# Optimization experiments

Hardware: AMD Instinct MI355X
Metric: run time of the kernel (lower is better)

## Reference

```python
import jax, jax.numpy as jnp
import numpy as np

B, J, D = 512, 22, 3
HIDDEN = 512
OUT = J * D          # 66, flattened frame size
NCLS = 12
LENGTH = 64


def setup_inputs() -> dict:
    key = jax.random.key(0)
    ks = jax.random.split(key, 12)
    s = 0.05
    return {
        "inputs": jax.random.normal(ks[0], (B, J, D), dtype=jnp.float32),
        "labels": jax.random.randint(ks[1], (B,), 0, NCLS),
        "length": LENGTH,
        # LSTMCell params (torch layout: W_ih [4H, in], W_hh [4H, H], gate order i,f,g,o)
        "W_ih": jax.random.normal(ks[2], (4 * HIDDEN, OUT + NCLS), dtype=jnp.float32) * s,
        "W_hh": jax.random.normal(ks[3], (4 * HIDDEN, HIDDEN), dtype=jnp.float32) * s,
        "b_ih": jax.random.normal(ks[4], (4 * HIDDEN,), dtype=jnp.float32) * s,
        "b_hh": jax.random.normal(ks[5], (4 * HIDDEN,), dtype=jnp.float32) * s,
        # fc: hidden -> output
        "W_fc": jax.random.normal(ks[6], (OUT, HIDDEN), dtype=jnp.float32) * s,
        "b_fc": jax.random.normal(ks[7], (OUT,), dtype=jnp.float32) * s,
        # fc_inh / fc_inc: output -> hidden (initial state projections)
        "W_inh": jax.random.normal(ks[8], (HIDDEN, OUT), dtype=jnp.float32) * s,
        "b_inh": jax.random.normal(ks[9], (HIDDEN,), dtype=jnp.float32) * s,
        "W_inc": jax.random.normal(ks[10], (HIDDEN, OUT), dtype=jnp.float32) * s,
        "b_inc": jax.random.normal(ks[11], (HIDDEN,), dtype=jnp.float32) * s,
    }


def reference(inputs, labels, length, W_ih, W_hh, b_ih, b_hh, W_fc, b_fc,
              W_inh, b_inh, W_inc, b_inc):
    b, j, d = inputs.shape
    enc = jax.nn.one_hot(labels, NCLS, dtype=inputs.dtype)      # [B, NCLS]
    frame0 = inputs.reshape(b, j * d)                            # [B, OUT]
    h0 = frame0 @ W_inh.T + b_inh                                # [B, H]
    c0 = frame0 @ W_inc.T + b_inc                                # [B, H]
    frame = jnp.concatenate([frame0, enc], axis=-1)              # [B, OUT+NCLS]

    def step(carry, _):
        h, c, fr = carry
        gates = fr @ W_ih.T + b_ih + h @ W_hh.T + b_hh           # [B, 4H]
        i, f, g, o = jnp.split(gates, 4, axis=-1)                # torch gate order
        c_new = jax.nn.sigmoid(f) * c + jax.nn.sigmoid(i) * jnp.tanh(g)
        h_new = jax.nn.sigmoid(o) * jnp.tanh(c_new)
        out = h_new @ W_fc.T + b_fc                              # [B, OUT]
        fr_new = jnp.concatenate([out, enc], axis=-1)
        return (h_new, c_new, fr_new), out

    _, outs = jax.lax.scan(step, (h0, c0, frame), None, length=length)  # [L, B, OUT]
    return jnp.transpose(outs, (1, 0, 2)).reshape(b, length, j, d)
```

## Files before the change

### kernel.cpp

```cpp
#include <hip/hip_runtime.h>

#define OUTD 66
#define INW  78
#define FH   2048
#define LEN  64

typedef short bf16x8 __attribute__((ext_vector_type(8)));
typedef float f32x4  __attribute__((ext_vector_type(4)));
typedef unsigned int u32x4 __attribute__((ext_vector_type(4)));

__device__ __forceinline__ float bf2f(unsigned short u) {
  union { unsigned int i; float f; } v; v.i = ((unsigned int)u) << 16; return v.f;
}
__device__ __forceinline__ unsigned short f2bf(float f) {
  union { float f; unsigned int i; } v; v.f = f;
  unsigned int u = v.i;
  return (unsigned short)((u + 0x7fffu + ((u >> 16) & 1u)) >> 16);
}
__device__ __forceinline__ float sigm(float x) { return 1.f / (1.f + __expf(-x)); }
__device__ __forceinline__ float tanh_f(float x) { return 2.f / (1.f + __expf(-2.f * x)) - 1.f; }

__device__ __forceinline__ unsigned int atom_add_ret(unsigned int* p, unsigned int d) {
  unsigned int r;
  asm volatile("global_atomic_add %0, %1, %2, off sc0\n\ts_waitcnt vmcnt(0)"
               : "=&v"(r) : "v"(p), "v"(d) : "memory");
  return r;
}

__global__ __launch_bounds__(256) void k_initA(
    const float* __restrict__ W_hh, const float* __restrict__ W_ih,
    const float* __restrict__ W_fc, const float* __restrict__ b_ih,
    const float* __restrict__ b_hh, const float* __restrict__ b_fc,
    const float* __restrict__ inp, const float* __restrict__ W_inh,
    const float* __restrict__ b_inh, const float* __restrict__ W_inc,
    const float* __restrict__ b_inc,
    unsigned short* __restrict__ Weff, float* __restrict__ bias_eff,
    unsigned short* __restrict__ hbuf, float* __restrict__ c0,
    unsigned short* __restrict__ Wfc16, unsigned int* __restrict__ flags,
    unsigned int* __restrict__ flagsL)
{
  int tid = threadIdx.x, bid = blockIdx.x;
  if (bid < 256) {
    int nb = bid;
    int k = tid * 2;
    float acc[8][2];
    #pragma unroll
    for (int r = 0; r < 8; ++r) {
      int n = nb * 8 + r;
      acc[r][0] = W_hh[n * 512 + k];
      acc[r][1] = W_hh[n * 512 + k + 1];
    }
    for (int m = 0; m < OUTD; ++m) {
      float w0 = W_fc[m * 512 + k];
      float w1 = W_fc[m * 512 + k + 1];
      #pragma unroll
      for (int r = 0; r < 8; ++r) {
        float wih = W_ih[(nb * 8 + r) * INW + m];
        acc[r][0] += wih * w0;
        acc[r][1] += wih * w1;
      }
    }
    #pragma unroll
    for (int r = 0; r < 8; ++r) {
      int n = nb * 8 + r;
      unsigned int pack = (unsigned int)f2bf(acc[r][0]) | ((unsigned int)f2bf(acc[r][1]) << 16);
      *(unsigned int*)(Weff + n * 512 + k) = pack;
    }
    if (tid < 8) {
      int n = nb * 8 + tid;
      float a = b_ih[n] + b_hh[n];
      for (int m = 0; m < OUTD; ++m) a += b_fc[m] * W_ih[n * INW + m];
      bias_eff[n] = a;
    }
    if (nb == 0) {
      for (int i = tid; i < 512 * 16; i += 256) flags[i] = 0;
      for (int i = tid; i < 256 * 16; i += 256) flagsL[i] = 0;
    }
  } else {
    int nb = bid - 256;
    for (int r = 0; r < 2; ++r) {
      int b = nb * 2 + r;
      for (int half = 0; half < 2; ++half) {
        int c = tid + half * 256;
        float ha = b_inh[c], ca = b_inc[c];
        for (int m = 0; m < OUTD; ++m) {
          float f = inp[b * OUTD + m];
          ha += f * W_inh[c * OUTD + m];
          ca += f * W_inc[c * OUTD + m];
        }
        hbuf[((b >> 5) * 32 + (c >> 4)) * 512 + (b & 31) * 16 + (c & 15)] = f2bf(ha);
        c0[b * 512 + c] = ca;
      }
    }
    if (nb == 0) {
      for (int i = tid; i < OUTD * 512; i += 256) Wfc16[i] = f2bf(W_fc[i]);
    }
  }
}

__global__ __launch_bounds__(128) void k_init2a(
    const float* __restrict__ inp, const unsigned short* __restrict__ hbuf,
    const float* __restrict__ W_fc, const float* __restrict__ b_fc,
    float* __restrict__ d0)
{
  int b = blockIdx.x, m = threadIdx.x;
  if (m >= OUTD) return;
  const unsigned short* hb = hbuf + (b >> 5) * 16384 + (b & 31) * 16;
  const float* wrow = W_fc + m * 512;
  float acc = 0.f;
  for (int k = 0; k < 512; ++k)
    acc += bf2f(hb[(k >> 4) * 512 + (k & 15)]) * wrow[k];
  d0[b * OUTD + m] = inp[b * OUTD + m] - (acc + b_fc[m]);
}

__global__ __launch_bounds__(256) void k_init2b(
    const float* __restrict__ d0, const float* __restrict__ W_ih,
    float* __restrict__ corr0)
{
  __shared__ float ds[4][OUTD];
  int tid = threadIdx.x, b0 = blockIdx.x * 4;
  for (int i = tid; i < 4 * OUTD; i += 256) ds[i / OUTD][i % OUTD] = d0[b0 * OUTD + i];
  __syncthreads();
  for (int n = tid; n < FH; n += 256) {
    float a0 = 0, a1 = 0, a2 = 0, a3 = 0;
    const float* wr = W_ih + n * INW;
    for (int m = 0; m < OUTD; ++m) {
      float w = wr[m];
      a0 += ds[0][m] * w; a1 += ds[1][m] * w; a2 += ds[2][m] * w; a3 += ds[3][m] * w;
    }
    corr0[(b0 + 0) * FH + n] = a0;
    corr0[(b0 + 1) * FH + n] = a1;
    corr0[(b0 + 2) * FH + n] = a2;
    corr0[(b0 + 3) * FH + n] = a3;
  }
}

__global__ __launch_bounds__(256, 2) void k_main(
    const unsigned short* __restrict__ Weff, const float* __restrict__ bias_eff,
    unsigned short* __restrict__ hbuf, const float* __restrict__ c0,
    const float* __restrict__ corr0, const float* __restrict__ W_ih,
    const int* __restrict__ labels, const unsigned short* __restrict__ Wfc16,
    const float* __restrict__ b_fc, float* __restrict__ out,
    unsigned int* __restrict__ flags, unsigned int* __restrict__ flagsL)
{
  __shared__ __align__(16) unsigned short h_lds[32 * 512];

  int tid = threadIdx.x, bid = blockIdx.x;
  int w = tid >> 6, lane = tid & 63;
  int lc = lane & 15, kg = lane >> 4;
  unsigned int* xmap = flags + 4608;
  unsigned int* decp = flags + 4100;

  unsigned int xcd;
  asm volatile("s_getreg_b32 %0, hwreg(HW_REG_XCC_ID)" : "=s"(xcd));
  if (tid == 0)
    __hip_atomic_store(&xmap[bid * 4], xcd + 1u, __ATOMIC_RELAXED, __HIP_MEMORY_SCOPE_AGENT);

  if (bid == 0 && w == 0) {
    int okA = 1, okB = 1;
    #pragma unroll
    for (int i = 0; i < 8; ++i) {
      int b = lane + i * 64;
      unsigned int v, ra, rb;
      const unsigned int* xp = &xmap[b * 4];
      for (;;) { v = __hip_atomic_load(xp, __ATOMIC_RELAXED, __HIP_MEMORY_SCOPE_AGENT);
                 if (v) break; __builtin_amdgcn_s_sleep(1); }
      const unsigned int* pa = &xmap[(b & 15) * 4];
      for (;;) { ra = __hip_atomic_load(pa, __ATOMIC_RELAXED, __HIP_MEMORY_SCOPE_AGENT);
                 if (ra) break; __builtin_amdgcn_s_sleep(1); }
      const unsigned int* pb = &xmap[((b >> 5) << 5) * 4];
      for (;;) { rb = __hip_atomic_load(pb, __ATOMIC_RELAXED, __HIP_MEMORY_SCOPE_AGENT);
                 if (rb) break; __builtin_amdgcn_s_sleep(1); }
      okA &= (v == ra); okB &= (v == rb);
    }
    okA = __all(okA); okB = __all(okB);
    if (lane == 0) {
      unsigned int d = okA ? 1u : (okB ? 2u : 3u);
      __hip_atomic_store(decp, d, __ATOMIC_RELAXED, __HIP_MEMORY_SCOPE_AGENT);
    }
  }
  if (tid == 0) {
    unsigned int dd;
    for (;;) { dd = __hip_atomic_load(decp, __ATOMIC_RELAXED, __HIP_MEMORY_SCOPE_AGENT);
               if (dd) break; __builtin_amdgcn_s_sleep(1); }
    h_lds[0] = (unsigned short)dd;
  }
  __syncthreads();
  unsigned int dmode = h_lds[0];
  __syncthreads();

  int fast, mt, jt;
  if (dmode == 1u)      { fast = 1; mt = bid & 15;  jt = bid >> 4; }
  else if (dmode == 2u) { fast = 1; mt = bid >> 5;  jt = bid & 31; }
  else                  { fast = 0; mt = bid & 15;  jt = bid >> 4; }

  int row0 = mt * 32, j0 = jt * 16;
  int hx0 = (w >> 1) * 8;
  int xloc = lc & 7;
  int G = lc >> 3;
  int hcol = j0 + hx0 + xloc;
  int rw0 = (w & 1) * 16;

  int sA = xloc;
  int tA16 = ((kg ^ sA) & 3) << 4;
  int ue64 = ((sA >> 2) & 1) << 6;
  int ub128 = ((lc >> 3) & 1) << 7;
  int PA0 = (rw0 + lc) * 1024 + tA16 + ue64 + ub128;
  int PF  = ((w & 1) * 16 + lc) * 1024 + tA16 + ue64 + ub128;

  bf16x8 Bfrag[16][2];
  #pragma unroll
  for (int cg = 0; cg < 2; ++cg) {
    int n = (cg * 2 + G) * 512 + hcol;
    const unsigned short* p = Weff + n * 512 + kg * 8;
    #pragma unroll
    for (int i = 0; i < 16; ++i) Bfrag[i][cg] = *(const bf16x8*)(p + i * 32);
  }

  bf16x8 Wf[16];
  float fcb = 0.f;
  int dofcW = (jt < 5) & (w < 2);
  {
    int n = j0 + lc;
    if (dofcW && n < OUTD) {
      const unsigned short* p = Wfc16 + n * 512 + kg * 8;
      #pragma unroll
      for (int i = 0; i < 16; ++i) Wf[i] = *(const bf16x8*)(p + i * 32);
      fcb = b_fc[n];
    } else {
      bf16x8 z8 = {0, 0, 0, 0, 0, 0, 0, 0};
      #pragma unroll
      for (int i = 0; i < 16; ++i) Wf[i] = z8;
    }
  }

  int qsel = G * 2;
  float lt[4][2], creg[2];
  #pragma unroll
  for (int idx = 0; idx < 2; ++idx) {
    int rloc = rw0 + kg * 4 + qsel + idx;
    int grow = row0 + rloc;
    int lab = labels[grow];
    #pragma unroll
    for (int gt = 0; gt < 4; ++gt) {
      int n = gt * 512 + hcol;
      lt[gt][idx] = bias_eff[n] + W_ih[n * INW + OUTD + lab];
    }
    creg[idx] = c0[grow * 512 + hcol];
  }

  const f32x4 z = {0.f, 0.f, 0.f, 0.f};
  unsigned int* myflag = &flags[(mt * 32 + jt) * 8];
  int agentMode = !fast;

  {
    const unsigned short* hsrc = hbuf + mt * 16384;
    #pragma unroll
    for (int i = 0; i < 8; ++i) {
      int n = tid + i * 256;
      int c = n >> 6, q = n & 63;
      int r = q >> 1, u = q & 1, g = c * 2 + u;
      *(u32x4*)(h_lds + r * 512 + ((g ^ (r & 15)) << 3)) =
          *(const u32x4*)(hsrc + n * 8);
    }
  }
  __syncthreads();

  f32x4 faP = z; int havP = 0, colP = 0;

  for (int s = 0; s < LEN; ++s) {
    if (havP) {
      int c = j0 + lc;
      if (c < OUTD) {
        #pragma unroll
        for (int q = 0; q < 4; ++q) {
          int b = row0 + (w & 1) * 16 + kg * 4 + q;
          out[((long)b * 64 + colP) * OUTD + c] = faP[q] + fcb;
        }
      }
      havP = 0;
    }

    f32x4 acc00 = z, acc01 = z;
    #pragma unroll
    for (int i = 0; i < 16; ++i) {
      bf16x8 a0 = *(const bf16x8*)((const char*)h_lds + (PA0 ^ (i << 6)));
      acc00 = __builtin_amdgcn_mfma_f32_16x16x32_bf16(a0, Bfrag[i][0], acc00, 0, 0, 0);
      acc01 = __builtin_amdgcn_mfma_f32_16x16x32_bf16(a0, Bfrag[i][1], acc01, 0, 0, 0);
    }

    f32x4 sh00, sh01;
    #pragma unroll
    for (int j = 0; j < 4; ++j) {
      sh00[j] = __shfl_xor(acc00[j], 8);
      sh01[j] = __shfl_xor(acc01[j], 8);
    }

    unsigned short hval[2];
    #pragma unroll
    for (int idx = 0; idx < 2; ++idx) {
      int qo = qsel + idx;
      float xi = (G ? sh00[qo] : acc00[qo]);
      float xf = (G ? acc00[qo] : sh00[qo]);
      float xg = (G ? sh01[qo] : acc01[qo]);
      float xo = (G ? acc01[qo] : sh01[qo]);
      xi += lt[0][idx]; xf += lt[1][idx]; xg += lt[2][idx]; xo += lt[3][idx];
      if (s == 0) {
        int rloc = rw0 + kg * 4 + qo;
        const float* cr = corr0 + (long)(row0 + rloc) * FH + hcol;
        xi += cr[0]; xf += cr[512]; xg += cr[1024]; xo += cr[1536];
      }
      float cn = sigm(xf) * creg[idx] + sigm(xi) * tanh_f(xg);
      creg[idx] = cn;
      hval[idx] = f2bf(sigm(xo) * tanh_f(cn));
    }

    {
      unsigned int* hdst32 = (unsigned int*)(hbuf + ((s + 1) & 1) * 262144);
      int base32 = (mt * 32 + jt) * 256;
      int ceL = (hx0 >> 1) + (xloc >> 1);
      int odd = xloc & 1;
      unsigned int pkS = 0; int rlS = 0;
      #pragma unroll
      for (int idx = 0; idx < 2; ++idx) {
        unsigned int mine = hval[idx];
        unsigned int part = (unsigned int)__shfl_xor((int)mine, 1);
        unsigned int p = odd ? (part | (mine << 16)) : (mine | (part << 16));
        if (idx == odd) { pkS = p; rlS = rw0 + kg * 4 + qsel + idx; }
      }
      if (fast) {
        hdst32[base32 + rlS * 8 + ceL] = pkS;
      } else {
        __hip_atomic_store(&hdst32[base32 + rlS * 8 + ceL], pkS,
                           __ATOMIC_RELAXED, __HIP_MEMORY_SCOPE_AGENT);
      }
    }

    __builtin_amdgcn_s_waitcnt(0);
    __syncthreads();
    if (tid == 128) {
      if (fast) {
        unsigned int* cntp = &flagsL[mt * 64 + ((s + 1) & 3)];
        unsigned int old = atom_add_ret(cntp, 1u);
        if (old == 31u) {
          *(volatile unsigned int*)&flagsL[mt * 64 + 32 + ((s + 1) & 3)] =
              (unsigned int)(s + 1);
          *(volatile unsigned int*)&flagsL[mt * 64 + ((s + 3) & 3)] = 0u;
        }
      }
      __hip_atomic_store(myflag, (unsigned int)(s + 1),
                         __ATOMIC_RELAXED, __HIP_MEMORY_SCOPE_AGENT);
    }

    if (dofcW && s >= 1) {
      f32x4 fa = z;
      #pragma unroll
      for (int i = 0; i < 16; ++i) {
        bf16x8 a = *(const bf16x8*)((const char*)h_lds + (PF ^ (i << 6)));
        fa = __builtin_amdgcn_mfma_f32_16x16x32_bf16(a, Wf[i], fa, 0, 0, 0);
      }
      faP = fa; havP = 1; colP = s - 1;
    }

    int needE = (s < LEN - 1) || (jt < 5);
    if (w == 3 && needE) {
      if (!agentMode) {
        volatile const unsigned int* gop =
            (volatile const unsigned int*)&flagsL[mt * 64 + 32 + ((s + 1) & 3)];
        int spins = 0;
        for (;;) {
          asm volatile("buffer_inv\n\ts_waitcnt vmcnt(0)" ::: "memory");
          if (*gop == (unsigned int)(s + 1)) break;
          if (++spins > 1024) { agentMode = 1; break; }
          __builtin_amdgcn_s_sleep(1);
        }
      }
      if (agentMode) {
        const unsigned int* fA = flags + (mt * 32 + (lane & 31)) * 8;
        for (;;) {
          unsigned int fv = __hip_atomic_load(fA, __ATOMIC_RELAXED, __HIP_MEMORY_SCOPE_AGENT);
          if (__all((int)(fv >= (unsigned int)(s + 1)))) break;
          __builtin_amdgcn_s_sleep(1);
        }
      }
    }
    __syncthreads();

    if (needE) {
      if (fast) {
        asm volatile("buffer_inv\n\ts_waitcnt vmcnt(0)" ::: "memory");
      } else {
        __builtin_amdgcn_fence(__ATOMIC_ACQUIRE, "agent");
      }
      const unsigned short* hbC = hbuf + ((s + 1) & 1) * 262144 + mt * 16384;
      u32x4 ta[8];
      #pragma unroll
      for (int i = 0; i < 8; ++i) {
        const unsigned short* cp = hbC + (w * 8 + i) * 512 + lane * 8;
        ta[i] = *(const u32x4*)cp;
      }
      int r_ = lane >> 1, u = lane & 1;
      #pragma unroll
      for (int i = 0; i < 8; ++i) {
        int c2 = (w * 8 + i) * 2 + u;
        *(u32x4*)(h_lds + r_ * 512 + ((c2 ^ (r_ & 15)) << 3)) = ta[i];
      }
    }
    __syncthreads();
  }

  if (dofcW) {
    int c = j0 + lc;
    if (havP && c < OUTD) {
      #pragma unroll
      for (int q = 0; q < 4; ++q) {
        int b = row0 + (w & 1) * 16 + kg * 4 + q;
        out[((long)b * 64 + colP) * OUTD + c] = faP[q] + fcb;
      }
    }
    f32x4 fa = z;
    #pragma unroll
    for (int i = 0; i < 16; ++i) {
      bf16x8 a = *(const bf16x8*)((const char*)h_lds + (PF ^ (i << 6)));
      fa = __builtin_amdgcn_mfma_f32_16x16x32_bf16(a, Wf[i], fa, 0, 0, 0);
    }
    if (c < OUTD) {
      #pragma unroll
      for (int q = 0; q < 4; ++q) {
        int b = row0 + (w & 1) * 16 + kg * 4 + q;
        out[((long)b * 64 + 63) * OUTD + c] = fa[q] + fcb;
      }
    }
  }
}

extern "C" void kernel_launch(void* const* d_in, const int* in_sizes, int n_in,
                              void* d_out, int out_size, void* d_ws, size_t ws_size,
                              hipStream_t stream) {
  (void)in_sizes; (void)n_in; (void)out_size; (void)ws_size;
  const float* inp   = (const float*)d_in[0];
  const int*   labels= (const int*)d_in[1];
  const float* W_ih  = (const float*)d_in[3];
  const float* W_hh  = (const float*)d_in[4];
  const float* b_ih  = (const float*)d_in[5];
  const float* b_hh  = (const float*)d_in[6];
  const float* W_fc  = (const float*)d_in[7];
  const float* b_fc  = (const float*)d_in[8];
  const float* W_inh = (const float*)d_in[9];
  const float* b_inh = (const float*)d_in[10];
  const float* W_inc = (const float*)d_in[11];
  const float* b_inc = (const float*)d_in[12];

  char* ws = (char*)d_ws;
  unsigned short* Weff = (unsigned short*)(ws + 0);
  float* bias_eff      = (float*)(ws + 2097152);
  unsigned short* hbuf = (unsigned short*)(ws + 2105344);
  float* c0            = (float*)(ws + 3153920);
  float* corr0         = (float*)(ws + 4202496);
  float* d0            = (float*)(ws + 8396800);
  unsigned int* flags  = (unsigned int*)(ws + 8531968);
  unsigned short* Wfc16= (unsigned short*)(ws + 8564736);
  unsigned int* flagsL = (unsigned int*)(ws + 8632320);

  k_initA<<<512, 256, 0, stream>>>(W_hh, W_ih, W_fc, b_ih, b_hh, b_fc,
                                   inp, W_inh, b_inh, W_inc, b_inc,
                                   Weff, bias_eff, hbuf, c0, Wfc16, flags, flagsL);
  k_init2a<<<512, 128, 0, stream>>>(inp, hbuf, W_fc, b_fc, d0);
  k_init2b<<<128, 256, 0, stream>>>(d0, W_ih, corr0);

  k_main<<<512, 256, 0, stream>>>(Weff, bias_eff, hbuf, c0, corr0, W_ih, labels,
                                  Wfc16, b_fc, (float*)d_out, flags, flagsL);
}
```

Before: 444.6 us.

## Use hierarchical barrier counters, overlap output stores, rebalance h reload across waves

The single 32-way atomic counter per row tile becomes a two-level tree: four sub-counters of eight blocks each, then a top counter of four, to reduce atomic contention in the grid barrier. Output stores for the previous step move to after the h writes, and the wait before the barrier leaves the four output stores outstanding instead of draining all memory ops. In blocks with jt<5 the h reload from global memory shifts to waves 2 and 3 so that waves 0 and 1, which also run the fc matmul, do less of it. The LDS swizzle changes from r&15 to r&7 with the matching read offset removed. The two-level barrier adds an extra atomic round trip on the critical path.

```diff
diff --git a/kernel.cpp b/kernel.cpp
--- a/kernel.cpp
+++ b/kernel.cpp
@@ -204,9 +204,8 @@
   int sA = xloc;
   int tA16 = ((kg ^ sA) & 3) << 4;
   int ue64 = ((sA >> 2) & 1) << 6;
-  int ub128 = ((lc >> 3) & 1) << 7;
-  int PA0 = (rw0 + lc) * 1024 + tA16 + ue64 + ub128;
-  int PF  = ((w & 1) * 16 + lc) * 1024 + tA16 + ue64 + ub128;
+  int PA0 = (rw0 + lc) * 1024 + tA16 + ue64;
+  int PF  = ((w & 1) * 16 + lc) * 1024 + tA16 + ue64;
 
   bf16x8 Bfrag[16][2];
   #pragma unroll
@@ -251,6 +250,7 @@
 
   const f32x4 z = {0.f, 0.f, 0.f, 0.f};
   unsigned int* myflag = &flags[(mt * 32 + jt) * 8];
+  unsigned int* gbase = flagsL + mt * 256;
   int agentMode = !fast;
 
   {
@@ -260,7 +260,7 @@
       int n = tid + i * 256;
       int c = n >> 6, q = n & 63;
       int r = q >> 1, u = q & 1, g = c * 2 + u;
-      *(u32x4*)(h_lds + r * 512 + ((g ^ (r & 15)) << 3)) =
+      *(u32x4*)(h_lds + r * 512 + ((g ^ (r & 7)) << 3)) =
           *(const u32x4*)(hsrc + n * 8);
     }
   }
@@ -269,18 +269,6 @@
   f32x4 faP = z; int havP = 0, colP = 0;
 
   for (int s = 0; s < LEN; ++s) {
-    if (havP) {
-      int c = j0 + lc;
-      if (c < OUTD) {
-        #pragma unroll
-        for (int q = 0; q < 4; ++q) {
-          int b = row0 + (w & 1) * 16 + kg * 4 + q;
-          out[((long)b * 64 + colP) * OUTD + c] = faP[q] + fcb;
-        }
-      }
-      havP = 0;
-    }
-
     f32x4 acc00 = z, acc01 = z;
     #pragma unroll
     for (int i = 0; i < 16; ++i) {
@@ -335,17 +323,40 @@
                            __ATOMIC_RELAXED, __HIP_MEMORY_SCOPE_AGENT);
       }
     }
-
-    __builtin_amdgcn_s_waitcnt(0);
+    asm volatile("" ::: "memory");
+
+    int hadOut = havP;
+    if (havP) {
+      int c = j0 + lc;
+      if (c < OUTD) {
+        #pragma unroll
+        for (int q = 0; q < 4; ++q) {
+          int b = row0 + (w & 1) * 16 + kg * 4 + q;
+          out[((long)b * 64 + colP) * OUTD + c] = faP[q] + fcb;
+        }
+      }
+      havP = 0;
+    }
+    asm volatile("" ::: "memory");
+
+    if (hadOut) asm volatile("s_waitcnt vmcnt(4) lgkmcnt(0)" ::: "memory");
+    else        asm volatile("s_waitcnt vmcnt(0) lgkmcnt(0)" ::: "memory");
     __syncthreads();
     if (tid == 128) {
       if (fast) {
-        unsigned int* cntp = &flagsL[mt * 64 + ((s + 1) & 3)];
-        unsigned int old = atom_add_ret(cntp, 1u);
-        if (old == 31u) {
-          *(volatile unsigned int*)&flagsL[mt * 64 + 32 + ((s + 1) & 3)] =
-              (unsigned int)(s + 1);
-          *(volatile unsigned int*)&flagsL[mt * 64 + ((s + 3) & 3)] = 0u;
+        int slot = (s + 1) & 3;
+        unsigned int so = atom_add_ret(gbase + 16 * (1 + (jt & 3)) + slot, 1u);
+        if (so == 7u) {
+          unsigned int mo = atom_add_ret(gbase + slot, 1u);
+          if (mo == 3u) {
+            *(volatile unsigned int*)(gbase + 80 + slot) = (unsigned int)(s + 1);
+            int zs = (s + 3) & 3;
+            *(volatile unsigned int*)(gbase + zs) = 0u;
+            *(volatile unsigned int*)(gbase + 16 + zs) = 0u;
+            *(volatile unsigned int*)(gbase + 32 + zs) = 0u;
+            *(volatile unsigned int*)(gbase + 48 + zs) = 0u;
+            *(volatile unsigned int*)(gbase + 64 + zs) = 0u;
+          }
         }
       }
       __hip_atomic_store(myflag, (unsigned int)(s + 1),
@@ -366,7 +377,7 @@
     if (w == 3 && needE) {
       if (!agentMode) {
         volatile const unsigned int* gop =
-            (volatile const unsigned int*)&flagsL[mt * 64 + 32 + ((s + 1) & 3)];
+            (volatile const unsigned int*)(gbase + 80 + ((s + 1) & 3));
         int spins = 0;
         for (;;) {
           asm volatile("buffer_inv\n\ts_waitcnt vmcnt(0)" ::: "memory");
@@ -387,23 +398,30 @@
     __syncthreads();
 
     if (needE) {
-      if (fast) {
-        asm volatile("buffer_inv\n\ts_waitcnt vmcnt(0)" ::: "memory");
-      } else {
-        __builtin_amdgcn_fence(__ATOMIC_ACQUIRE, "agent");
-      }
-      const unsigned short* hbC = hbuf + ((s + 1) & 1) * 262144 + mt * 16384;
-      u32x4 ta[8];
-      #pragma unroll
-      for (int i = 0; i < 8; ++i) {
-        const unsigned short* cp = hbC + (w * 8 + i) * 512 + lane * 8;
-        ta[i] = *(const u32x4*)cp;
-      }
-      int r_ = lane >> 1, u = lane & 1;
-      #pragma unroll
-      for (int i = 0; i < 8; ++i) {
-        int c2 = (w * 8 + i) * 2 + u;
-        *(u32x4*)(h_lds + r_ * 512 + ((c2 ^ (r_ & 15)) << 3)) = ta[i];
+      int nhalf, cb;
+      if (jt < 5) { nhalf = (w >> 1) ? 2 : 0; cb = (w & 1) * 16; }
+      else        { nhalf = 1; cb = w * 8; }
+      if (nhalf) {
+        if (fast) {
+          asm volatile("buffer_inv\n\ts_waitcnt vmcnt(0)" ::: "memory");
+        } else {
+          __builtin_amdgcn_fence(__ATOMIC_ACQUIRE, "agent");
+        }
+        const unsigned short* hbC = hbuf + ((s + 1) & 1) * 262144 + mt * 16384;
+        for (int hf = 0; hf < nhalf; ++hf) {
+          u32x4 ta[8];
+          #pragma unroll
+          for (int i = 0; i < 8; ++i) {
+            int ci = cb + hf * 8 + i;
+            ta[i] = *(const u32x4*)(hbC + ci * 512 + lane * 8);
+          }
+          int r_ = lane >> 1, u = lane & 1;
+          #pragma unroll
+          for (int i = 0; i < 8; ++i) {
+            int c2 = (cb + hf * 8 + i) * 2 + u;
+            *(u32x4*)(h_lds + r_ * 512 + ((c2 ^ (r_ & 7)) << 3)) = ta[i];
+          }
+        }
       }
     }
     __syncthreads();
```

Measured after the change: 634.2 us. +42.6%, slower.
